# Kernel optimization log

Measured on AMD Instinct MI355X. Metric: run time of the kernel, lower is better.

Reference implementation:

```python
import jax, jax.numpy as jnp
import numpy as np

D_K = 64
SCALE = D_K ** (-0.5)
B, H, S = 2, 16, 2048


def setup_inputs() -> dict:
    key = jax.random.key(0)
    kq, kk, kv = jax.random.split(key, 3)
    q = jax.random.normal(kq, (B, H, S, D_K), dtype=jnp.float32)
    k = jax.random.normal(kk, (B, H, S, D_K), dtype=jnp.float32)
    v = jax.random.normal(kv, (B, H, S, D_K), dtype=jnp.float32)
    # causal mask: True means masked (matches torch masked_fill semantics)
    mask = jnp.triu(jnp.ones((S, S), dtype=bool), k=1)[None, None]  # [1,1,S,S]
    return {"q": q, "k": k, "v": v, "mask": mask}


def reference(q, k, v, mask) -> jnp.ndarray:
    # scores = q @ k^T  -> [B,H,S,S]
    scores = jnp.einsum("bhqd,bhkd->bhqk", q, k)
    # masked_fill(mask, -inf), then scale (as written in the source),
    # then softmax over the key axis. -inf * scale stays -inf.
    scores = jnp.where(mask, -jnp.inf, scores)
    attn = jax.nn.softmax(SCALE * scores, axis=-1)
    return jnp.einsum("bhqk,bhkd->bhqd", attn, v)
```

## Files before the change

kernel.cpp:

```cpp
#include <hip/hip_runtime.h>
#include <hip/hip_bf16.h>
#include <math.h>


constexpr int S  = 2048;
constexpr int D  = 64;
constexpr int BH = 32;
constexpr float SCALE = 0.125f;
constexpr float LOG2E = 1.4426950408889634f;
constexpr float QPRE  = SCALE * LOG2E;
constexpr int PSTR = 72;

typedef __attribute__((ext_vector_type(8))) short bf16x8;
typedef __attribute__((ext_vector_type(4))) short bf16x4;
typedef __attribute__((ext_vector_type(4))) float f32x4;

#if __has_builtin(__builtin_amdgcn_mfma_f32_16x16x16bf16_1k)
#define HAS_MFMA_1K 1
#else
#define HAS_MFMA_1K 0
#endif

#if __has_builtin(__builtin_amdgcn_exp2f)
#define EXP2F(x) __builtin_amdgcn_exp2f(x)
#else
#define EXP2F(x) exp2f(x)
#endif

__device__ __forceinline__ short f2bf(float x) {
    union { __hip_bfloat16 b; short s; } u; u.b = __float2bfloat16(x); return u.s;
}

__device__ __forceinline__ void gload_lds16(const void* g, void* lds) {
    __builtin_amdgcn_global_load_lds(
        (const __attribute__((address_space(1))) unsigned int*)g,
        (__attribute__((address_space(3))) unsigned int*)lds, 16, 0, 0);
}

__global__ __launch_bounds__(256) void preconv_25993142075924(
    const float* __restrict__ Kg, const float* __restrict__ Vg,
    short* __restrict__ Kb, short* __restrict__ VT)
{
    const int kt = blockIdx.x, bh = blockIdx.y, tid = threadIdx.x;
    __shared__ float lt[64 * 65];
    const float* kp = Kg + (size_t)bh * S * D;
    const float* vp = Vg + (size_t)bh * S * D;
    short* kb = Kb + (size_t)bh * S * D;
    short* vt = VT + (size_t)bh * D * S;
    #pragma unroll
    for (int e = 0; e < 4; ++e) {
        int idx = (tid + e * 256) * 4;
        int r = idx >> 6, c = idx & 63;
        f32x4 k4 = *(const f32x4*)(kp + (size_t)(kt * 64 + r) * D + c);
        bf16x4 kb4;
        kb4[0] = f2bf(k4[0]); kb4[1] = f2bf(k4[1]);
        kb4[2] = f2bf(k4[2]); kb4[3] = f2bf(k4[3]);
        *(bf16x4*)(kb + (size_t)(kt * 64 + r) * D + c) = kb4;
        f32x4 v4 = *(const f32x4*)(vp + (size_t)(kt * 64 + r) * D + c);
        lt[(c + 0) * 65 + r] = v4[0];
        lt[(c + 1) * 65 + r] = v4[1];
        lt[(c + 2) * 65 + r] = v4[2];
        lt[(c + 3) * 65 + r] = v4[3];
    }
    __syncthreads();
    #pragma unroll
    for (int e = 0; e < 2; ++e) {
        int tt = tid + e * 256;
        int d  = tt >> 3;
        int j0 = (tt & 7) * 8;
        bf16x8 o;
        #pragma unroll
        for (int jj = 0; jj < 8; ++jj)
            o[jj] = f2bf(lt[d * 65 + j0 + jj]);
        *(bf16x8*)(vt + (size_t)d * S + kt * 64 + j0) = o;
    }
}

__global__ __launch_bounds__(256, 3) void attn_fwd_v8_25993142075924(
    const float* __restrict__ Qg, const short* __restrict__ Kb,
    const short* __restrict__ VT, float* __restrict__ Og)
{
    const int bh  = blockIdx.x;
    const int qb  = 31 - (int)blockIdx.y;
    const int tid = threadIdx.x;
    const int wv  = tid >> 6;
    const int ln  = tid & 63;
    const int c16 = ln & 15;
    const int qd  = ln >> 4;

    const int q0  = qb * 64 + wv * 16;
    const int nkt = qb + 1;

    __shared__ __align__(16) short lk[2][64 * 64];
    __shared__ __align__(16) short lv[2][64 * 64];
#if !HAS_MFMA_1K
    __shared__ __align__(16) short lp[4 * 16 * PSTR];
    short* lpw = lp + wv * 16 * PSTR;
#endif

    const float* qp = Qg + (size_t)bh * S * D;
    const short* kp = Kb + (size_t)bh * S * D;
    const short* vp = VT + (size_t)bh * D * S;
    float*       op = Og + (size_t)bh * S * D;

    const int srow0 = wv * 16 + (ln >> 3);
    const int sgrp0 = (ln & 7) ^ (srow0 & 7);
    const int srow1 = srow0 + 8;
    const int sgrp1 = (ln & 7) ^ (srow1 & 7);

    bf16x8 qf[2];
    {
        const float* src = qp + (size_t)(q0 + c16) * D + qd * 8;
        #pragma unroll
        for (int khf = 0; khf < 2; ++khf) {
            f32x4 a = *(const f32x4*)(src + khf * 32);
            f32x4 b = *(const f32x4*)(src + khf * 32 + 4);
            bf16x8 f;
            f[0] = f2bf(a[0] * QPRE); f[1] = f2bf(a[1] * QPRE);
            f[2] = f2bf(a[2] * QPRE); f[3] = f2bf(a[3] * QPRE);
            f[4] = f2bf(b[0] * QPRE); f[5] = f2bf(b[1] * QPRE);
            f[6] = f2bf(b[2] * QPRE); f[7] = f2bf(b[3] * QPRE);
            qf[khf] = f;
        }
    }

    f32x4 oacc[4] = {{0,0,0,0},{0,0,0,0},{0,0,0,0},{0,0,0,0}};
    float lsum = 0.f;

    gload_lds16(kp + (size_t)srow0 * D + sgrp0 * 8, &lk[0][(wv * 16 + 0) * 64]);
    gload_lds16(vp + (size_t)srow0 * S + sgrp0 * 8, &lv[0][(wv * 16 + 0) * 64]);
    gload_lds16(kp + (size_t)srow1 * D + sgrp1 * 8, &lk[0][(wv * 16 + 8) * 64]);
    gload_lds16(vp + (size_t)srow1 * S + sgrp1 * 8, &lv[0][(wv * 16 + 8) * 64]);
    __syncthreads();

    for (int kt = 0; kt < nkt; ++kt) {
        const int cur = kt & 1;
        if (kt + 1 < nkt) {
            const int nxt = cur ^ 1;
            const size_t kb0 = (size_t)(kt + 1) * 64;
            gload_lds16(kp + (kb0 + srow0) * D + sgrp0 * 8, &lk[nxt][(wv * 16 + 0) * 64]);
            gload_lds16(vp + (size_t)srow0 * S + kb0 + sgrp0 * 8, &lv[nxt][(wv * 16 + 0) * 64]);
            gload_lds16(kp + (kb0 + srow1) * D + sgrp1 * 8, &lk[nxt][(wv * 16 + 8) * 64]);
            gload_lds16(vp + (size_t)srow1 * S + kb0 + sgrp1 * 8, &lv[nxt][(wv * 16 + 8) * 64]);
        }

#if HAS_MFMA_1K
        bf16x4 vf[4][4];
        #pragma unroll
        for (int dt = 0; dt < 4; ++dt) {
            const int row = dt * 16 + c16;
            #pragma unroll
            for (int nt = 0; nt < 4; ++nt) {
                const int gl = nt * 2 + (qd >> 1);
                const int gp = gl ^ (c16 & 7);
                vf[dt][nt] = *(const bf16x4*)&lv[cur][row * 64 + gp * 8 + (qd & 1) * 4];
            }
        }
#endif

        float t[4][4];
        #pragma unroll
        for (int nt = 0; nt < 4; ++nt) {
            const int row = nt * 16 + c16;
            f32x4 acc = {0,0,0,0};
            #pragma unroll
            for (int khf = 0; khf < 2; ++khf) {
                const int g = (khf * 4 + qd) ^ (row & 7);
                bf16x8 kf = *(const bf16x8*)&lk[cur][row * 64 + g * 8];
                acc = __builtin_amdgcn_mfma_f32_16x16x32_bf16(kf, qf[khf], acc, 0, 0, 0);
            }
            t[nt][0] = acc[0]; t[nt][1] = acc[1]; t[nt][2] = acc[2]; t[nt][3] = acc[3];
        }

        if (kt == qb) {
            #pragma unroll
            for (int nt = 0; nt < 4; ++nt) {
                #pragma unroll
                for (int r = 0; r < 4; ++r) {
                    int key = kt * 64 + nt * 16 + qd * 4 + r;
                    if (key > q0 + c16) t[nt][r] = -INFINITY;
                }
            }
        }

        float pval[4][4];
        #pragma unroll
        for (int nt = 0; nt < 4; ++nt)
            #pragma unroll
            for (int r = 0; r < 4; ++r) {
                float pv = EXP2F(t[nt][r]);
                pval[nt][r] = pv;
                lsum += pv;
            }

#if HAS_MFMA_1K
        #pragma unroll
        for (int nt = 0; nt < 4; ++nt) {
            bf16x4 pf;
            pf[0] = f2bf(pval[nt][0]); pf[1] = f2bf(pval[nt][1]);
            pf[2] = f2bf(pval[nt][2]); pf[3] = f2bf(pval[nt][3]);
            #pragma unroll
            for (int dt = 0; dt < 4; ++dt)
                oacc[dt] = __builtin_amdgcn_mfma_f32_16x16x16bf16_1k(
                    vf[dt][nt], pf, oacc[dt], 0, 0, 0);
        }
#else
        #pragma unroll
        for (int nt = 0; nt < 4; ++nt)
            #pragma unroll
            for (int r = 0; r < 4; ++r)
                lpw[c16 * PSTR + nt * 16 + qd * 4 + r] = f2bf(pval[nt][r]);
        bf16x8 pf2[2];
        #pragma unroll
        for (int khf = 0; khf < 2; ++khf)
            pf2[khf] = *(const bf16x8*)&lpw[c16 * PSTR + khf * 32 + qd * 8];
        #pragma unroll
        for (int dt = 0; dt < 4; ++dt) {
            const int row = dt * 16 + c16;
            #pragma unroll
            for (int khf = 0; khf < 2; ++khf) {
                const int g = (khf * 4 + qd) ^ (row & 7);
                bf16x8 vf8 = *(const bf16x8*)&lv[cur][row * 64 + g * 8];
                oacc[dt] = __builtin_amdgcn_mfma_f32_16x16x32_bf16(vf8, pf2[khf], oacc[dt], 0, 0, 0);
            }
        }
#endif

        __syncthreads();
    }

    float s = lsum;
    s += __shfl_xor(s, 16);
    s += __shfl_xor(s, 32);
    const float inv = 1.0f / s;
    float* dst = op + (size_t)(q0 + c16) * D;
    #pragma unroll
    for (int dt = 0; dt < 4; ++dt) {
        f32x4 o;
        o[0] = oacc[dt][0] * inv; o[1] = oacc[dt][1] * inv;
        o[2] = oacc[dt][2] * inv; o[3] = oacc[dt][3] * inv;
        *(f32x4*)(dst + dt * 16 + qd * 4) = o;
    }
}

__global__ __launch_bounds__(256) void attn_fwd_v1_25993142075924(
    const float* __restrict__ Qg, const float* __restrict__ Kg,
    const float* __restrict__ Vg, float* __restrict__ Og)
{
    constexpr int KSTR = 72;
    constexpr int BQ = 64, BK = 64;
    const int qt  = blockIdx.x;
    const int bh  = blockIdx.y;
    const int tid = threadIdx.x;
    const int wv  = tid >> 6;
    const int ln  = tid & 63;
    const int c16 = ln & 15;
    const int qd  = ln >> 4;

    __shared__ __align__(16) __hip_bfloat16 lk [BK][KSTR];
    __shared__ __align__(16) __hip_bfloat16 lvt[D ][KSTR];
    __shared__ __align__(16) __hip_bfloat16 lp [4][16][KSTR];

    const size_t hoff = (size_t)bh * S * D;
    const float* qp = Qg + hoff;
    const float* kp = Kg + hoff;
    const float* vp = Vg + hoff;
    float*       op = Og + hoff;
    const int q0 = qt * BQ;

    bf16x8 qf[2];
    {
        const float* src = qp + (size_t)(q0 + wv*16 + c16) * D + qd*8;
        #pragma unroll
        for (int kh = 0; kh < 2; ++kh) {
            f32x4 a = *(const f32x4*)(src + kh*32);
            f32x4 b = *(const f32x4*)(src + kh*32 + 4);
            bf16x8 f;
            f[0]=f2bf(a[0]*QPRE); f[1]=f2bf(a[1]*QPRE); f[2]=f2bf(a[2]*QPRE); f[3]=f2bf(a[3]*QPRE);
            f[4]=f2bf(b[0]*QPRE); f[5]=f2bf(b[1]*QPRE); f[6]=f2bf(b[2]*QPRE); f[7]=f2bf(b[3]*QPRE);
            qf[kh] = f;
        }
    }

    f32x4 oacc[4] = {{0,0,0,0},{0,0,0,0},{0,0,0,0},{0,0,0,0}};
    float mrun[4] = {-INFINITY,-INFINITY,-INFINITY,-INFINITY};
    float lrun[4] = {0.f,0.f,0.f,0.f};

    const int nkt = qt + 1;
    for (int kt = 0; kt < nkt; ++kt) {
        __syncthreads();
        #pragma unroll
        for (int e = 0; e < 4; ++e) {
            int idx = (tid + e*256) * 4;
            int row = idx >> 6, col = idx & 63;
            f32x4 k4 = *(const f32x4*)(kp + (size_t)(kt*BK + row)*D + col);
            bf16x4 kb;
            kb[0]=f2bf(k4[0]); kb[1]=f2bf(k4[1]); kb[2]=f2bf(k4[2]); kb[3]=f2bf(k4[3]);
            *(bf16x4*)&lk[row][col] = kb;
            f32x4 v4 = *(const f32x4*)(vp + (size_t)(kt*BK + row)*D + col);
            lvt[col+0][row] = __float2bfloat16(v4[0]);
            lvt[col+1][row] = __float2bfloat16(v4[1]);
            lvt[col+2][row] = __float2bfloat16(v4[2]);
            lvt[col+3][row] = __float2bfloat16(v4[3]);
        }
        __syncthreads();

        float t[4][4];
        #pragma unroll
        for (int nt = 0; nt < 4; ++nt) {
            f32x4 acc = {0,0,0,0};
            #pragma unroll
            for (int kh = 0; kh < 2; ++kh) {
                bf16x8 kf = *(const bf16x8*)&lk[nt*16 + c16][kh*32 + qd*8];
                acc = __builtin_amdgcn_mfma_f32_16x16x32_bf16(qf[kh], kf, acc, 0, 0, 0);
            }
            #pragma unroll
            for (int r = 0; r < 4; ++r) t[nt][r] = acc[r];
        }
        if (kt == nkt - 1) {
            #pragma unroll
            for (int nt = 0; nt < 4; ++nt) {
                int j = kt*BK + nt*16 + c16;
                #pragma unroll
                for (int r = 0; r < 4; ++r)
                    if (j > q0 + wv*16 + qd*4 + r) t[nt][r] = -INFINITY;
            }
        }

        float pval[4][4];
        #pragma unroll
        for (int r = 0; r < 4; ++r) {
            float tm = fmaxf(fmaxf(t[0][r], t[1][r]), fmaxf(t[2][r], t[3][r]));
            tm = fmaxf(tm, __shfl_xor(tm, 1));
            tm = fmaxf(tm, __shfl_xor(tm, 2));
            tm = fmaxf(tm, __shfl_xor(tm, 4));
            tm = fmaxf(tm, __shfl_xor(tm, 8));
            float mnew  = fmaxf(mrun[r], tm);
            float alpha = exp2f(mrun[r] - mnew);
            mrun[r] = mnew;
            float rs = 0.f;
            #pragma unroll
            for (int nt = 0; nt < 4; ++nt) {
                float pv = exp2f(t[nt][r] - mnew);
                pval[nt][r] = pv;
                rs += pv;
            }
            rs += __shfl_xor(rs, 1);
            rs += __shfl_xor(rs, 2);
            rs += __shfl_xor(rs, 4);
            rs += __shfl_xor(rs, 8);
            lrun[r] = lrun[r] * alpha + rs;
            #pragma unroll
            for (int dt = 0; dt < 4; ++dt) oacc[dt][r] *= alpha;
        }

        #pragma unroll
        for (int nt = 0; nt < 4; ++nt)
            #pragma unroll
            for (int r = 0; r < 4; ++r)
                lp[wv][qd*4 + r][nt*16 + c16] = __float2bfloat16(pval[nt][r]);
        bf16x8 pf[2];
        #pragma unroll
        for (int kh = 0; kh < 2; ++kh)
            pf[kh] = *(const bf16x8*)&lp[wv][c16][kh*32 + qd*8];

        #pragma unroll
        for (int dt = 0; dt < 4; ++dt) {
            #pragma unroll
            for (int kh = 0; kh < 2; ++kh) {
                bf16x8 vf = *(const bf16x8*)&lvt[dt*16 + c16][kh*32 + qd*8];
                oacc[dt] = __builtin_amdgcn_mfma_f32_16x16x32_bf16(pf[kh], vf, oacc[dt], 0, 0, 0);
            }
        }
    }

    #pragma unroll
    for (int r = 0; r < 4; ++r) {
        float inv = 1.0f / lrun[r];
        float* dst = op + (size_t)(q0 + wv*16 + qd*4 + r) * D;
        #pragma unroll
        for (int dt = 0; dt < 4; ++dt)
            dst[dt*16 + c16] = oacc[dt][r] * inv;
    }
}

extern "C" void kernel_launch(void* const* d_in, const int* in_sizes, int n_in,
                              void* d_out, int out_size, void* d_ws, size_t ws_size,
                              hipStream_t stream) {
    const float* q = (const float*)d_in[0];
    const float* k = (const float*)d_in[1];
    const float* v = (const float*)d_in[2];
    float* out = (float*)d_out;
    const size_t elems = (size_t)BH * S * D;
    const size_t need  = 2 * elems * sizeof(short);
    if (ws_size >= need) {
        short* Kb = (short*)d_ws;
        short* VT = Kb + elems;
        preconv_25993142075924<<<dim3(S / 64, BH), 256, 0, stream>>>(k, v, Kb, VT);
        attn_fwd_v8_25993142075924<<<dim3(BH, 32), 256, 0, stream>>>(q, Kb, VT, out);
    } else {
        attn_fwd_v1_25993142075924<<<dim3(S / 64, BH), 256, 0, stream>>>(q, k, v, out);
    }
}
```

Measured before the change: 135.7 us.

## Use 512-thread blocks covering 128 query rows to share K/V tile loads

Each workgroup now handles 128 query rows with 8 waves instead of 64 rows with 4 waves. Every K/V tile loaded into LDS is reused by twice as many waves, which halves the per-thread load work and the total number of tile loads. Waves in the lower half skip compute on the final diagonal tile but still take part in loads and barriers. The trade-offs are idle waves on the last tile, fewer blocks to balance the causal triangle across, and larger barrier groups.

```diff
diff --git a/kernel.cpp b/kernel.cpp
--- a/kernel.cpp
+++ b/kernel.cpp
@@ -76,25 +76,26 @@
     }
 }
 
-__global__ __launch_bounds__(256, 3) void attn_fwd_v8_25993142075924(
+__global__ __launch_bounds__(512, 4) void attn_fwd_v9_25993142075924(
     const float* __restrict__ Qg, const short* __restrict__ Kb,
     const short* __restrict__ VT, float* __restrict__ Og)
 {
     const int bh  = blockIdx.x;
-    const int qb  = 31 - (int)blockIdx.y;
+    const int p   = 15 - (int)blockIdx.y;
     const int tid = threadIdx.x;
     const int wv  = tid >> 6;
     const int ln  = tid & 63;
     const int c16 = ln & 15;
     const int qd  = ln >> 4;
 
-    const int q0  = qb * 64 + wv * 16;
-    const int nkt = qb + 1;
+    const int q0  = p * 128 + wv * 16;
+    const int qbw = 2 * p + (wv >> 2);
+    const int nkt = 2 * p + 2;
 
     __shared__ __align__(16) short lk[2][64 * 64];
     __shared__ __align__(16) short lv[2][64 * 64];
 #if !HAS_MFMA_1K
-    __shared__ __align__(16) short lp[4 * 16 * PSTR];
+    __shared__ __align__(16) short lp[8 * 16 * PSTR];
     short* lpw = lp + wv * 16 * PSTR;
 #endif
 
@@ -103,10 +104,8 @@
     const short* vp = VT + (size_t)bh * D * S;
     float*       op = Og + (size_t)bh * S * D;
 
-    const int srow0 = wv * 16 + (ln >> 3);
-    const int sgrp0 = (ln & 7) ^ (srow0 & 7);
-    const int srow1 = srow0 + 8;
-    const int sgrp1 = (ln & 7) ^ (srow1 & 7);
+    const int srow = wv * 8 + (ln >> 3);
+    const int sgrp = (ln & 7) ^ (srow & 7);
 
     bf16x8 qf[2];
     {
@@ -127,10 +126,8 @@
     f32x4 oacc[4] = {{0,0,0,0},{0,0,0,0},{0,0,0,0},{0,0,0,0}};
     float lsum = 0.f;
 
-    gload_lds16(kp + (size_t)srow0 * D + sgrp0 * 8, &lk[0][(wv * 16 + 0) * 64]);
-    gload_lds16(vp + (size_t)srow0 * S + sgrp0 * 8, &lv[0][(wv * 16 + 0) * 64]);
-    gload_lds16(kp + (size_t)srow1 * D + sgrp1 * 8, &lk[0][(wv * 16 + 8) * 64]);
-    gload_lds16(vp + (size_t)srow1 * S + sgrp1 * 8, &lv[0][(wv * 16 + 8) * 64]);
+    gload_lds16(kp + (size_t)srow * D + sgrp * 8, &lk[0][(wv * 8) * 64]);
+    gload_lds16(vp + (size_t)srow * S + sgrp * 8, &lv[0][(wv * 8) * 64]);
     __syncthreads();
 
     for (int kt = 0; kt < nkt; ++kt) {
@@ -138,93 +135,93 @@
         if (kt + 1 < nkt) {
             const int nxt = cur ^ 1;
             const size_t kb0 = (size_t)(kt + 1) * 64;
-            gload_lds16(kp + (kb0 + srow0) * D + sgrp0 * 8, &lk[nxt][(wv * 16 + 0) * 64]);
-            gload_lds16(vp + (size_t)srow0 * S + kb0 + sgrp0 * 8, &lv[nxt][(wv * 16 + 0) * 64]);
-            gload_lds16(kp + (kb0 + srow1) * D + sgrp1 * 8, &lk[nxt][(wv * 16 + 8) * 64]);
-            gload_lds16(vp + (size_t)srow1 * S + kb0 + sgrp1 * 8, &lv[nxt][(wv * 16 + 8) * 64]);
-        }
-
+            gload_lds16(kp + (kb0 + srow) * D + sgrp * 8, &lk[nxt][(wv * 8) * 64]);
+            gload_lds16(vp + (size_t)srow * S + kb0 + sgrp * 8, &lv[nxt][(wv * 8) * 64]);
+        }
+
+        if (kt <= qbw) {
 #if HAS_MFMA_1K
-        bf16x4 vf[4][4];
-        #pragma unroll
-        for (int dt = 0; dt < 4; ++dt) {
-            const int row = dt * 16 + c16;
+            bf16x4 vf[4][4];
+            #pragma unroll
+            for (int dt = 0; dt < 4; ++dt) {
+                const int row = dt * 16 + c16;
+                #pragma unroll
+                for (int nt = 0; nt < 4; ++nt) {
+                    const int gl = nt * 2 + (qd >> 1);
+                    const int gp = gl ^ (c16 & 7);
+                    vf[dt][nt] = *(const bf16x4*)&lv[cur][row * 64 + gp * 8 + (qd & 1) * 4];
+                }
+            }
+#endif
+
+            float t[4][4];
             #pragma unroll
             for (int nt = 0; nt < 4; ++nt) {
-                const int gl = nt * 2 + (qd >> 1);
-                const int gp = gl ^ (c16 & 7);
-                vf[dt][nt] = *(const bf16x4*)&lv[cur][row * 64 + gp * 8 + (qd & 1) * 4];
-            }
-        }
+                const int row = nt * 16 + c16;
+                f32x4 acc = {0,0,0,0};
+                #pragma unroll
+                for (int khf = 0; khf < 2; ++khf) {
+                    const int g = (khf * 4 + qd) ^ (row & 7);
+                    bf16x8 kf = *(const bf16x8*)&lk[cur][row * 64 + g * 8];
+                    acc = __builtin_amdgcn_mfma_f32_16x16x32_bf16(kf, qf[khf], acc, 0, 0, 0);
+                }
+                t[nt][0] = acc[0]; t[nt][1] = acc[1]; t[nt][2] = acc[2]; t[nt][3] = acc[3];
+            }
+
+            if (kt == qbw) {
+                #pragma unroll
+                for (int nt = 0; nt < 4; ++nt) {
+                    #pragma unroll
+                    for (int r = 0; r < 4; ++r) {
+                        int key = kt * 64 + nt * 16 + qd * 4 + r;
+                        if (key > q0 + c16) t[nt][r] = -INFINITY;
+                    }
+                }
+            }
+
+            float pval[4][4];
+            #pragma unroll
+            for (int nt = 0; nt < 4; ++nt)
+                #pragma unroll
+                for (int r = 0; r < 4; ++r) {
+                    float pv = EXP2F(t[nt][r]);
+                    pval[nt][r] = pv;
+                    lsum += pv;
+                }
+
+#if HAS_MFMA_1K
+            #pragma unroll
+            for (int nt = 0; nt < 4; ++nt) {
+                bf16x4 pf;
+                pf[0] = f2bf(pval[nt][0]); pf[1] = f2bf(pval[nt][1]);
+                pf[2] = f2bf(pval[nt][2]); pf[3] = f2bf(pval[nt][3]);
+                #pragma unroll
+                for (int dt = 0; dt < 4; ++dt)
+                    oacc[dt] = __builtin_amdgcn_mfma_f32_16x16x16bf16_1k(
+                        vf[dt][nt], pf, oacc[dt], 0, 0, 0);
+            }
+#else
+            #pragma unroll
+            for (int nt = 0; nt < 4; ++nt)
+                #pragma unroll
+                for (int r = 0; r < 4; ++r)
+                    lpw[c16 * PSTR + nt * 16 + qd * 4 + r] = f2bf(pval[nt][r]);
+            bf16x8 pf2[2];
+            #pragma unroll
+            for (int khf = 0; khf < 2; ++khf)
+                pf2[khf] = *(const bf16x8*)&lpw[c16 * PSTR + khf * 32 + qd * 8];
+            #pragma unroll
+            for (int dt = 0; dt < 4; ++dt) {
+                const int row = dt * 16 + c16;
+                #pragma unroll
+                for (int khf = 0; khf < 2; ++khf) {
+                    const int g = (khf * 4 + qd) ^ (row & 7);
+                    bf16x8 vf8 = *(const bf16x8*)&lv[cur][row * 64 + g * 8];
+                    oacc[dt] = __builtin_amdgcn_mfma_f32_16x16x32_bf16(vf8, pf2[khf], oacc[dt], 0, 0, 0);
+                }
+            }
 #endif
-
-        float t[4][4];
-        #pragma unroll
-        for (int nt = 0; nt < 4; ++nt) {
-            const int row = nt * 16 + c16;
-            f32x4 acc = {0,0,0,0};
-            #pragma unroll
-            for (int khf = 0; khf < 2; ++khf) {
-                const int g = (khf * 4 + qd) ^ (row & 7);
-                bf16x8 kf = *(const bf16x8*)&lk[cur][row * 64 + g * 8];
-                acc = __builtin_amdgcn_mfma_f32_16x16x32_bf16(kf, qf[khf], acc, 0, 0, 0);
-            }
-            t[nt][0] = acc[0]; t[nt][1] = acc[1]; t[nt][2] = acc[2]; t[nt][3] = acc[3];
-        }
-
-        if (kt == qb) {
-            #pragma unroll
-            for (int nt = 0; nt < 4; ++nt) {
-                #pragma unroll
-                for (int r = 0; r < 4; ++r) {
-                    int key = kt * 64 + nt * 16 + qd * 4 + r;
-                    if (key > q0 + c16) t[nt][r] = -INFINITY;
-                }
-            }
-        }
-
-        float pval[4][4];
-        #pragma unroll
-        for (int nt = 0; nt < 4; ++nt)
-            #pragma unroll
-            for (int r = 0; r < 4; ++r) {
-                float pv = EXP2F(t[nt][r]);
-                pval[nt][r] = pv;
-                lsum += pv;
-            }
-
-#if HAS_MFMA_1K
-        #pragma unroll
-        for (int nt = 0; nt < 4; ++nt) {
-            bf16x4 pf;
-            pf[0] = f2bf(pval[nt][0]); pf[1] = f2bf(pval[nt][1]);
-            pf[2] = f2bf(pval[nt][2]); pf[3] = f2bf(pval[nt][3]);
-            #pragma unroll
-            for (int dt = 0; dt < 4; ++dt)
-                oacc[dt] = __builtin_amdgcn_mfma_f32_16x16x16bf16_1k(
-                    vf[dt][nt], pf, oacc[dt], 0, 0, 0);
-        }
-#else
-        #pragma unroll
-        for (int nt = 0; nt < 4; ++nt)
-            #pragma unroll
-            for (int r = 0; r < 4; ++r)
-                lpw[c16 * PSTR + nt * 16 + qd * 4 + r] = f2bf(pval[nt][r]);
-        bf16x8 pf2[2];
-        #pragma unroll
-        for (int khf = 0; khf < 2; ++khf)
-            pf2[khf] = *(const bf16x8*)&lpw[c16 * PSTR + khf * 32 + qd * 8];
-        #pragma unroll
-        for (int dt = 0; dt < 4; ++dt) {
-            const int row = dt * 16 + c16;
-            #pragma unroll
-            for (int khf = 0; khf < 2; ++khf) {
-                const int g = (khf * 4 + qd) ^ (row & 7);
-                bf16x8 vf8 = *(const bf16x8*)&lv[cur][row * 64 + g * 8];
-                oacc[dt] = __builtin_amdgcn_mfma_f32_16x16x32_bf16(vf8, pf2[khf], oacc[dt], 0, 0, 0);
-            }
-        }
-#endif
+        }
 
         __syncthreads();
     }
@@ -397,7 +394,7 @@
         short* Kb = (short*)d_ws;
         short* VT = Kb + elems;
         preconv_25993142075924<<<dim3(S / 64, BH), 256, 0, stream>>>(k, v, Kb, VT);
-        attn_fwd_v8_25993142075924<<<dim3(BH, 32), 256, 0, stream>>>(q, Kb, VT, out);
+        attn_fwd_v9_25993142075924<<<dim3(BH, 16), 512, 0, stream>>>(q, Kb, VT, out);
     } else {
         attn_fwd_v1_25993142075924<<<dim3(S / 64, BH), 256, 0, stream>>>(q, k, v, out);
     }
```

Result: slower. 140.7 us (+3.6%).

## Process two 16-row query groups per wave with 128-thread blocks

Applied to the files above, without the earlier changes.

Blocks drop from four waves to two, and each wave now handles 32 query rows as two 16-row groups. K fragments are loaded from LDS once per key tile and reused across both query groups, which cuts LDS reads per MFMA. The cost is more accumulator registers per wave (two sets of output accumulators and Q fragments) and half as many waves per block, which may lower occupancy and latency hiding. Each wave also issues twice as many global-to-LDS copies to fill the tiles.

```diff
diff --git a/kernel.cpp b/kernel.cpp
--- a/kernel.cpp
+++ b/kernel.cpp
@@ -76,7 +76,7 @@
     }
 }
 
-__global__ __launch_bounds__(256, 3) void attn_fwd_v8_25993142075924(
+__global__ __launch_bounds__(128, 3) void attn_fwd_v10_25993142075924(
     const float* __restrict__ Qg, const short* __restrict__ Kb,
     const short* __restrict__ VT, float* __restrict__ Og)
 {
@@ -88,13 +88,13 @@
     const int c16 = ln & 15;
     const int qd  = ln >> 4;
 
-    const int q0  = qb * 64 + wv * 16;
+    const int q0  = qb * 64 + wv * 32;
     const int nkt = qb + 1;
 
     __shared__ __align__(16) short lk[2][64 * 64];
     __shared__ __align__(16) short lv[2][64 * 64];
 #if !HAS_MFMA_1K
-    __shared__ __align__(16) short lp[4 * 16 * PSTR];
+    __shared__ __align__(16) short lp[2 * 16 * PSTR];
     short* lpw = lp + wv * 16 * PSTR;
 #endif
 
@@ -103,14 +103,17 @@
     const short* vp = VT + (size_t)bh * D * S;
     float*       op = Og + (size_t)bh * S * D;
 
-    const int srow0 = wv * 16 + (ln >> 3);
-    const int sgrp0 = (ln & 7) ^ (srow0 & 7);
-    const int srow1 = srow0 + 8;
-    const int sgrp1 = (ln & 7) ^ (srow1 & 7);
-
-    bf16x8 qf[2];
-    {
-        const float* src = qp + (size_t)(q0 + c16) * D + qd * 8;
+    int srow[4], sgrp[4];
+    #pragma unroll
+    for (int i = 0; i < 4; ++i) {
+        srow[i] = wv * 32 + i * 8 + (ln >> 3);
+        sgrp[i] = (ln & 7) ^ (srow[i] & 7);
+    }
+
+    bf16x8 qf[2][2];
+    #pragma unroll
+    for (int qg = 0; qg < 2; ++qg) {
+        const float* src = qp + (size_t)(q0 + qg * 16 + c16) * D + qd * 8;
         #pragma unroll
         for (int khf = 0; khf < 2; ++khf) {
             f32x4 a = *(const f32x4*)(src + khf * 32);
@@ -120,17 +123,21 @@
             f[2] = f2bf(a[2] * QPRE); f[3] = f2bf(a[3] * QPRE);
             f[4] = f2bf(b[0] * QPRE); f[5] = f2bf(b[1] * QPRE);
             f[6] = f2bf(b[2] * QPRE); f[7] = f2bf(b[3] * QPRE);
-            qf[khf] = f;
-        }
-    }
-
-    f32x4 oacc[4] = {{0,0,0,0},{0,0,0,0},{0,0,0,0},{0,0,0,0}};
-    float lsum = 0.f;
-
-    gload_lds16(kp + (size_t)srow0 * D + sgrp0 * 8, &lk[0][(wv * 16 + 0) * 64]);
-    gload_lds16(vp + (size_t)srow0 * S + sgrp0 * 8, &lv[0][(wv * 16 + 0) * 64]);
-    gload_lds16(kp + (size_t)srow1 * D + sgrp1 * 8, &lk[0][(wv * 16 + 8) * 64]);
-    gload_lds16(vp + (size_t)srow1 * S + sgrp1 * 8, &lv[0][(wv * 16 + 8) * 64]);
+            qf[qg][khf] = f;
+        }
+    }
+
+    f32x4 oacc[2][4] = {{{0,0,0,0},{0,0,0,0},{0,0,0,0},{0,0,0,0}},
+                        {{0,0,0,0},{0,0,0,0},{0,0,0,0},{0,0,0,0}}};
+    float lsum[2] = {0.f, 0.f};
+
+    #pragma unroll
+    for (int i = 0; i < 4; ++i) {
+        gload_lds16(kp + (size_t)srow[i] * D + sgrp[i] * 8,
+                    &lk[0][(wv * 32 + i * 8) * 64]);
+        gload_lds16(vp + (size_t)srow[i] * S + sgrp[i] * 8,
+                    &lv[0][(wv * 32 + i * 8) * 64]);
+    }
     __syncthreads();
 
     for (int kt = 0; kt < nkt; ++kt) {
@@ -138,12 +145,25 @@
         if (kt + 1 < nkt) {
             const int nxt = cur ^ 1;
             const size_t kb0 = (size_t)(kt + 1) * 64;
-            gload_lds16(kp + (kb0 + srow0) * D + sgrp0 * 8, &lk[nxt][(wv * 16 + 0) * 64]);
-            gload_lds16(vp + (size_t)srow0 * S + kb0 + sgrp0 * 8, &lv[nxt][(wv * 16 + 0) * 64]);
-            gload_lds16(kp + (kb0 + srow1) * D + sgrp1 * 8, &lk[nxt][(wv * 16 + 8) * 64]);
-            gload_lds16(vp + (size_t)srow1 * S + kb0 + sgrp1 * 8, &lv[nxt][(wv * 16 + 8) * 64]);
-        }
-
+            #pragma unroll
+            for (int i = 0; i < 4; ++i) {
+                gload_lds16(kp + (kb0 + srow[i]) * D + sgrp[i] * 8,
+                            &lk[nxt][(wv * 32 + i * 8) * 64]);
+                gload_lds16(vp + (size_t)srow[i] * S + kb0 + sgrp[i] * 8,
+                            &lv[nxt][(wv * 32 + i * 8) * 64]);
+            }
+        }
+
+        bf16x8 kf[4][2];
+        #pragma unroll
+        for (int nt = 0; nt < 4; ++nt) {
+            const int row = nt * 16 + c16;
+            #pragma unroll
+            for (int khf = 0; khf < 2; ++khf) {
+                const int g = (khf * 4 + qd) ^ (row & 7);
+                kf[nt][khf] = *(const bf16x8*)&lk[cur][row * 64 + g * 8];
+            }
+        }
 #if HAS_MFMA_1K
         bf16x4 vf[4][4];
         #pragma unroll
@@ -158,88 +178,89 @@
         }
 #endif
 
-        float t[4][4];
-        #pragma unroll
-        for (int nt = 0; nt < 4; ++nt) {
-            const int row = nt * 16 + c16;
-            f32x4 acc = {0,0,0,0};
-            #pragma unroll
-            for (int khf = 0; khf < 2; ++khf) {
-                const int g = (khf * 4 + qd) ^ (row & 7);
-                bf16x8 kf = *(const bf16x8*)&lk[cur][row * 64 + g * 8];
-                acc = __builtin_amdgcn_mfma_f32_16x16x32_bf16(kf, qf[khf], acc, 0, 0, 0);
-            }
-            t[nt][0] = acc[0]; t[nt][1] = acc[1]; t[nt][2] = acc[2]; t[nt][3] = acc[3];
-        }
-
-        if (kt == qb) {
+        #pragma unroll
+        for (int qg = 0; qg < 2; ++qg) {
+            float t[4][4];
             #pragma unroll
             for (int nt = 0; nt < 4; ++nt) {
+                f32x4 acc = {0,0,0,0};
+                acc = __builtin_amdgcn_mfma_f32_16x16x32_bf16(kf[nt][0], qf[qg][0], acc, 0, 0, 0);
+                acc = __builtin_amdgcn_mfma_f32_16x16x32_bf16(kf[nt][1], qf[qg][1], acc, 0, 0, 0);
+                t[nt][0] = acc[0]; t[nt][1] = acc[1]; t[nt][2] = acc[2]; t[nt][3] = acc[3];
+            }
+
+            if (kt == qb) {
+                #pragma unroll
+                for (int nt = 0; nt < 4; ++nt) {
+                    #pragma unroll
+                    for (int r = 0; r < 4; ++r) {
+                        int key = kt * 64 + nt * 16 + qd * 4 + r;
+                        if (key > q0 + qg * 16 + c16) t[nt][r] = -INFINITY;
+                    }
+                }
+            }
+
+            float pval[4][4];
+            #pragma unroll
+            for (int nt = 0; nt < 4; ++nt)
                 #pragma unroll
                 for (int r = 0; r < 4; ++r) {
-                    int key = kt * 64 + nt * 16 + qd * 4 + r;
-                    if (key > q0 + c16) t[nt][r] = -INFINITY;
+                    float pv = EXP2F(t[nt][r]);
+                    pval[nt][r] = pv;
+                    lsum[qg] += pv;
                 }
-            }
-        }
-
-        float pval[4][4];
-        #pragma unroll
-        for (int nt = 0; nt < 4; ++nt)
-            #pragma unroll
-            for (int r = 0; r < 4; ++r) {
-                float pv = EXP2F(t[nt][r]);
-                pval[nt][r] = pv;
-                lsum += pv;
-            }
 
 #if HAS_MFMA_1K
-        #pragma unroll
-        for (int nt = 0; nt < 4; ++nt) {
-            bf16x4 pf;
-            pf[0] = f2bf(pval[nt][0]); pf[1] = f2bf(pval[nt][1]);
-            pf[2] = f2bf(pval[nt][2]); pf[3] = f2bf(pval[nt][3]);
-            #pragma unroll
-            for (int dt = 0; dt < 4; ++dt)
-                oacc[dt] = __builtin_amdgcn_mfma_f32_16x16x16bf16_1k(
-                    vf[dt][nt], pf, oacc[dt], 0, 0, 0);
-        }
+            #pragma unroll
+            for (int nt = 0; nt < 4; ++nt) {
+                bf16x4 pf;
+                pf[0] = f2bf(pval[nt][0]); pf[1] = f2bf(pval[nt][1]);
+                pf[2] = f2bf(pval[nt][2]); pf[3] = f2bf(pval[nt][3]);
+                #pragma unroll
+                for (int dt = 0; dt < 4; ++dt)
+                    oacc[qg][dt] = __builtin_amdgcn_mfma_f32_16x16x16bf16_1k(
+                        vf[dt][nt], pf, oacc[qg][dt], 0, 0, 0);
+            }
 #else
-        #pragma unroll
-        for (int nt = 0; nt < 4; ++nt)
-            #pragma unroll
-            for (int r = 0; r < 4; ++r)
-                lpw[c16 * PSTR + nt * 16 + qd * 4 + r] = f2bf(pval[nt][r]);
-        bf16x8 pf2[2];
-        #pragma unroll
-        for (int khf = 0; khf < 2; ++khf)
-            pf2[khf] = *(const bf16x8*)&lpw[c16 * PSTR + khf * 32 + qd * 8];
+            #pragma unroll
+            for (int nt = 0; nt < 4; ++nt)
+                #pragma unroll
+                for (int r = 0; r < 4; ++r)
+                    lpw[c16 * PSTR + nt * 16 + qd * 4 + r] = f2bf(pval[nt][r]);
+            bf16x8 pf2[2];
+            #pragma unroll
+            for (int khf = 0; khf < 2; ++khf)
+                pf2[khf] = *(const bf16x8*)&lpw[c16 * PSTR + khf * 32 + qd * 8];
+            #pragma unroll
+            for (int dt = 0; dt < 4; ++dt) {
+                const int row = dt * 16 + c16;
+                #pragma unroll
+                for (int khf = 0; khf < 2; ++khf) {
+                    const int g = (khf * 4 + qd) ^ (row & 7);
+                    bf16x8 vf8 = *(const bf16x8*)&lv[cur][row * 64 + g * 8];
+                    oacc[qg][dt] = __builtin_amdgcn_mfma_f32_16x16x32_bf16(vf8, pf2[khf], oacc[qg][dt], 0, 0, 0);
+                }
+            }
+#endif
+        }
+
+        __syncthreads();
+    }
+
+    #pragma unroll
+    for (int qg = 0; qg < 2; ++qg) {
+        float s = lsum[qg];
+        s += __shfl_xor(s, 16);
+        s += __shfl_xor(s, 32);
+        const float inv = 1.0f / s;
+        float* dst = op + (size_t)(q0 + qg * 16 + c16) * D;
         #pragma unroll
         for (int dt = 0; dt < 4; ++dt) {
-            const int row = dt * 16 + c16;
-            #pragma unroll
-            for (int khf = 0; khf < 2; ++khf) {
-                const int g = (khf * 4 + qd) ^ (row & 7);
-                bf16x8 vf8 = *(const bf16x8*)&lv[cur][row * 64 + g * 8];
-                oacc[dt] = __builtin_amdgcn_mfma_f32_16x16x32_bf16(vf8, pf2[khf], oacc[dt], 0, 0, 0);
-            }
-        }
-#endif
-
-        __syncthreads();
-    }
-
-    float s = lsum;
-    s += __shfl_xor(s, 16);
-    s += __shfl_xor(s, 32);
-    const float inv = 1.0f / s;
-    float* dst = op + (size_t)(q0 + c16) * D;
-    #pragma unroll
-    for (int dt = 0; dt < 4; ++dt) {
-        f32x4 o;
-        o[0] = oacc[dt][0] * inv; o[1] = oacc[dt][1] * inv;
-        o[2] = oacc[dt][2] * inv; o[3] = oacc[dt][3] * inv;
-        *(f32x4*)(dst + dt * 16 + qd * 4) = o;
+            f32x4 o;
+            o[0] = oacc[qg][dt][0] * inv; o[1] = oacc[qg][dt][1] * inv;
+            o[2] = oacc[qg][dt][2] * inv; o[3] = oacc[qg][dt][3] * inv;
+            *(f32x4*)(dst + dt * 16 + qd * 4) = o;
+        }
     }
 }
 
@@ -397,7 +418,7 @@
         short* Kb = (short*)d_ws;
         short* VT = Kb + elems;
         preconv_25993142075924<<<dim3(S / 64, BH), 256, 0, stream>>>(k, v, Kb, VT);
-        attn_fwd_v8_25993142075924<<<dim3(BH, 32), 256, 0, stream>>>(q, Kb, VT, out);
+        attn_fwd_v10_25993142075924<<<dim3(BH, 32), 128, 0, stream>>>(q, Kb, VT, out);
     } else {
         attn_fwd_v1_25993142075924<<<dim3(S / 64, BH), 256, 0, stream>>>(q, k, v, out);
     }
```

Measured after the change: 136.6 us. About the same (+0.7%).
